# Kernel optimization log

Hardware: AMD Instinct MI355X
Metric: run time of the kernel (lower is better)

Reference implementation:

```python
import jax, jax.numpy as jnp
import numpy as np

DIM = 1024
HEADS = 16


def setup_inputs() -> dict:
    key = jax.random.key(0)
    k1, k2, k3, k4 = jax.random.split(key, 4)
    x = jax.random.normal(k1, (4, 2048, DIM), dtype=jnp.float32)
    # torch nn.Linear weights: [out_features, in_features]
    w_qkv = jax.random.normal(k2, (3 * DIM, DIM), dtype=jnp.float32) * (DIM ** -0.5)
    w_out = jax.random.normal(k3, (DIM, DIM), dtype=jnp.float32) * (DIM ** -0.5)
    b_out = jax.random.normal(k4, (DIM,), dtype=jnp.float32) * 0.01
    return {"x": x, "w_qkv": w_qkv, "w_out": w_out, "b_out": b_out}


def reference(x, w_qkv, w_out, b_out):
    b, n, d = x.shape
    h = HEADS
    hd = d // h
    scale = d ** -0.5  # note: full dim, matching the original module
    qkv = jnp.einsum('bnd,ed->bne', x, w_qkv)  # [b, n, 3d]
    q, k, v = jnp.split(qkv, 3, axis=-1)
    def to_heads(t):
        return t.reshape(b, n, h, hd).transpose(0, 2, 1, 3)  # [b, h, n, hd]
    q, k, v = map(to_heads, (q, k, v))
    dots = jnp.einsum('bhqd,bhkd->bhqk', q, k) * scale  # [b, h, n, n]
    attn = jax.nn.softmax(dots, axis=-1)
    out = jnp.einsum('bhqk,bhkd->bhqd', attn, v)  # [b, h, n, hd]
    out = out.transpose(0, 2, 1, 3).reshape(b, n, d)
    return jnp.einsum('bnd,ed->bne', out, w_out) + b_out
```

## Files before the change

### kernel.cpp

```cpp
#include <hip/hip_runtime.h>
#include <stdint.h>

#define SEQ   2048
#define NDIM  1024
#define NH    16
#define HD    64
#define KDIM  1024

typedef short  short8  __attribute__((ext_vector_type(8)));
typedef float  floatx4 __attribute__((ext_vector_type(4)));
typedef unsigned short ushort4v __attribute__((ext_vector_type(4)));
typedef _Float16 half8 __attribute__((ext_vector_type(8)));
typedef __fp16  fp16x2 __attribute__((ext_vector_type(2)));
typedef unsigned int uint4v __attribute__((ext_vector_type(4)));

typedef __attribute__((address_space(1))) void GV;
typedef __attribute__((address_space(3))) void LV;

#define QSCALE 0.04508422003f

__device__ __forceinline__ unsigned short f2bf(float f) {
    unsigned int u = __float_as_uint(f);
    u += 0x7fffu + ((u >> 16) & 1u);
    return (unsigned short)(u >> 16);
}

__device__ __forceinline__ float ex2(float x) {
#if __has_builtin(__builtin_amdgcn_exp2f)
    return __builtin_amdgcn_exp2f(x);
#else
    return exp2f(x);
#endif
}

__global__ __launch_bounds__(256) void cast_f32_bf16(const float* __restrict__ in,
                                                     unsigned short* __restrict__ out) {
    int i = (blockIdx.x * 256 + threadIdx.x) * 4;
    float4 v = *(const float4*)(in + i);
    ushort4v o;
    o.x = f2bf(v.x); o.y = f2bf(v.y); o.z = f2bf(v.z); o.w = f2bf(v.w);
    *(ushort4v*)(out + i) = o;
}

template<int MODE>
__global__ __launch_bounds__(256, 3)
void gemm_bt(const unsigned short* __restrict__ A,
             const unsigned short* __restrict__ B,
             unsigned short* __restrict__ Cq,
             unsigned short* __restrict__ Ck,
             unsigned short* __restrict__ Cv,
             const float* __restrict__ bias,
             float* __restrict__ Cout)
{
    __shared__ unsigned short As[128 * 32];
    __shared__ unsigned short Bs[128 * 32];
    const int tid  = threadIdx.x;
    const int lane = tid & 63;
    const int w    = tid >> 6;
    const int quad = lane >> 4;
    const int l15  = lane & 15;
    const int wm   = w >> 1, wn = w & 1;
    const int bm   = blockIdx.x, bn = blockIdx.y;

    const unsigned short* Arow = A + (size_t)bm * 128 * KDIM;
    const unsigned short* Brow = B + (size_t)bn * 128 * KDIM;

    const unsigned short* ga[2]; const unsigned short* gb[2];
    unsigned short* la[2];       unsigned short* lb[2];
#pragma unroll
    for (int i = 0; i < 2; ++i) {
        int j = ((w * 2 + i) << 6) + lane;
        int r = j >> 2;
        int c = (j & 3) ^ ((r >> 1) & 3);
        ga[i] = Arow + r * KDIM + c * 8;
        gb[i] = Brow + r * KDIM + c * 8;
        la[i] = (unsigned short*)As + ((w * 2 + i) << 9);
        lb[i] = (unsigned short*)Bs + ((w * 2 + i) << 9);
    }

    int achunk[4], bchunk[4];
#pragma unroll
    for (int t = 0; t < 4; ++t) {
        int ra = wm * 64 + t * 16 + l15;
        achunk[t] = (ra << 2) + (quad ^ ((ra >> 1) & 3));
        int rb = wn * 64 + t * 16 + l15;
        bchunk[t] = (rb << 2) + (quad ^ ((rb >> 1) & 3));
    }

    floatx4 acc[4][4];
#pragma unroll
    for (int mt = 0; mt < 4; ++mt)
#pragma unroll
        for (int nt = 0; nt < 4; ++nt)
            acc[mt][nt] = (floatx4){0.f, 0.f, 0.f, 0.f};

    for (int kt = 0; kt < KDIM / 32; ++kt) {
#pragma unroll
        for (int i = 0; i < 2; ++i) {
            __builtin_amdgcn_global_load_lds((GV*)(void*)(ga[i] + kt * 32), (LV*)(void*)la[i], 16, 0, 0);
            __builtin_amdgcn_global_load_lds((GV*)(void*)(gb[i] + kt * 32), (LV*)(void*)lb[i], 16, 0, 0);
        }
        __syncthreads();
        short8 af[4], bf[4];
#pragma unroll
        for (int t = 0; t < 4; ++t) {
            af[t] = *(const short8*)(As + (achunk[t] << 3));
            bf[t] = *(const short8*)(Bs + (bchunk[t] << 3));
        }
#pragma unroll
        for (int mt = 0; mt < 4; ++mt)
#pragma unroll
            for (int nt = 0; nt < 4; ++nt)
                acc[mt][nt] = __builtin_amdgcn_mfma_f32_16x16x32_bf16(af[mt], bf[nt], acc[mt][nt], 0, 0, 0);
        __syncthreads();
    }

    if (MODE == 0) {
        const int which = bn >> 3;
        unsigned short* dst = which == 0 ? Cq : (which == 1 ? Ck : Cv);
#pragma unroll
        for (int nt = 0; nt < 4; ++nt) {
            int e0   = ((bn & 7) << 7) + wn * 64 + nt * 16;
            int head = e0 >> 6;
            int hdi  = (e0 & 63) + l15;
#pragma unroll
            for (int mt = 0; mt < 4; ++mt) {
#pragma unroll
                for (int r = 0; r < 4; ++r) {
                    int m = bm * 128 + wm * 64 + mt * 16 + quad * 4 + r;
                    int b = m >> 11, n = m & 2047;
                    int bh = (b << 4) + head;
                    float val = acc[mt][nt][r];
                    if (which == 0) {
                        dst[((size_t)bh * SEQ + n) * HD + hdi] = f2bf(val * QSCALE);
                    } else if (which == 1) {
                        size_t idx = (size_t)bh * 131072
                                   + (size_t)(n >> 7) * 8192
                                   + (size_t)((((n >> 4) & 7) * 2) + (hdi >> 5)) * 512
                                   + ((((hdi >> 3) & 3) * 16) + (n & 15)) * 8
                                   + (hdi & 7);
                        dst[idx] = f2bf(val);
                    } else {
                        int nt7 = n & 127;
                        int u   = nt7 >> 5;
                        int k5  = nt7 & 31;
                        int c   = k5 & 15;
                        int q   = c >> 2;
                        int j   = ((k5 >> 4) << 2) | (c & 3);
                        size_t idx = (size_t)bh * 131072
                                   + (size_t)(n >> 7) * 8192
                                   + (size_t)(u * 4 + ((hdi >> 4) & 3)) * 512
                                   + (q * 16 + (hdi & 15)) * 8
                                   + j;
                        _Float16 hv = (_Float16)val;
                        dst[idx] = __builtin_bit_cast(unsigned short, hv);
                    }
                }
            }
        }
    } else {
#pragma unroll
        for (int nt = 0; nt < 4; ++nt) {
            int e = bn * 128 + wn * 64 + nt * 16 + l15;
            float bv = bias[e];
#pragma unroll
            for (int mt = 0; mt < 4; ++mt) {
#pragma unroll
                for (int r = 0; r < 4; ++r) {
                    int m = bm * 128 + wm * 64 + mt * 16 + quad * 4 + r;
                    Cout[(size_t)m * NDIM + e] = acc[mt][nt][r] + bv;
                }
            }
        }
    }
}

__global__ __launch_bounds__(256, 4)
void attn_fused(const unsigned short* __restrict__ qb,
                const unsigned short* __restrict__ kfrag,
                const unsigned short* __restrict__ vfrag,
                unsigned short* __restrict__ ob)
{
    __shared__ unsigned short Ks[8192];
    __shared__ unsigned short Vs[8192];

    const int tid  = threadIdx.x;
    const int lane = tid & 63;
    const int w    = tid >> 6;
    const int quad = lane >> 4;
    const int l15  = lane & 15;

    const int bid  = blockIdx.x;
    const int xcd  = bid & 7;
    const int slot = bid >> 3;
    const int bh   = xcd * 8 + (slot >> 4);
    const int q0   = (slot & 15) * 128;

    const unsigned short* Qb = qb    + (size_t)bh * SEQ * HD;
    const unsigned short* Kb = kfrag + (size_t)bh * 131072;
    const unsigned short* Vb = vfrag + (size_t)bh * 131072;

    short8 qf[2][2];
#pragma unroll
    for (int qt = 0; qt < 2; ++qt)
#pragma unroll
        for (int ks = 0; ks < 2; ++ks)
            qf[qt][ks] = *(const short8*)(Qb + (size_t)(q0 + w * 32 + qt * 16 + l15) * HD + ks * 32 + quad * 8);

    floatx4 oacc[2][4];
    floatx4 lacc4[2];
#pragma unroll
    for (int qt = 0; qt < 2; ++qt) {
#pragma unroll
        for (int nt = 0; nt < 4; ++nt) oacc[qt][nt] = (floatx4){0.f, 0.f, 0.f, 0.f};
        lacc4[qt] = (floatx4){0.f, 0.f, 0.f, 0.f};
    }
    half8 vones;
#pragma unroll
    for (int i = 0; i < 8; ++i) vones[i] = (_Float16)1.0f;

    const unsigned short* gk[4]; const unsigned short* gv[4];
    unsigned short* lk[4];       unsigned short* lv[4];
#pragma unroll
    for (int i = 0; i < 4; ++i) {
        int chunk = ((w * 4 + i) << 6) + lane;
        gk[i] = Kb + chunk * 8;
        gv[i] = Vb + chunk * 8;
        lk[i] = (unsigned short*)Ks + ((w * 4 + i) << 9) + lane * 8;
        lv[i] = (unsigned short*)Vs + ((w * 4 + i) << 9) + lane * 8;
    }

    uint4v pk[4], pv[4];
#pragma unroll
    for (int i = 0; i < 4; ++i) {
        pk[i] = *(const uint4v*)gk[i];
        pv[i] = *(const uint4v*)gv[i];
    }

    for (int kt = 0; kt < 16; ++kt) {
#pragma unroll
        for (int i = 0; i < 4; ++i) {
            *(uint4v*)lk[i] = pk[i];
            *(uint4v*)lv[i] = pv[i];
        }
        __syncthreads();
        if (kt < 15) {
#pragma unroll
            for (int i = 0; i < 4; ++i) {
                pk[i] = *(const uint4v*)(gk[i] + (kt + 1) * 8192);
                pv[i] = *(const uint4v*)(gv[i] + (kt + 1) * 8192);
            }
        }

        floatx4 sacc[2][8];
#pragma unroll
        for (int qt = 0; qt < 2; ++qt)
#pragma unroll
            for (int nt = 0; nt < 8; ++nt) sacc[qt][nt] = (floatx4){0.f, 0.f, 0.f, 0.f};
#pragma unroll
        for (int ks = 0; ks < 2; ++ks) {
#pragma unroll
            for (int nt = 0; nt < 8; ++nt) {
                short8 kf = *(const short8*)(Ks + (nt * 2 + ks) * 512 + lane * 8);
                sacc[0][nt] = __builtin_amdgcn_mfma_f32_16x16x32_bf16(kf, qf[0][ks], sacc[0][nt], 0, 0, 0);
                sacc[1][nt] = __builtin_amdgcn_mfma_f32_16x16x32_bf16(kf, qf[1][ks], sacc[1][nt], 0, 0, 0);
            }
        }

#pragma unroll
        for (int u = 0; u < 4; ++u) {
            half8 pf[2];
#pragma unroll
            for (int qt = 0; qt < 2; ++qt) {
                floatx4 s0 = sacc[qt][2 * u];
                floatx4 s1 = sacc[qt][2 * u + 1];
                fp16x2 c0 = __builtin_amdgcn_cvt_pkrtz(ex2(s0[0]), ex2(s0[1]));
                fp16x2 c1 = __builtin_amdgcn_cvt_pkrtz(ex2(s0[2]), ex2(s0[3]));
                fp16x2 c2 = __builtin_amdgcn_cvt_pkrtz(ex2(s1[0]), ex2(s1[1]));
                fp16x2 c3 = __builtin_amdgcn_cvt_pkrtz(ex2(s1[2]), ex2(s1[3]));
                uint4v uu;
                uu.x = __builtin_bit_cast(unsigned int, c0);
                uu.y = __builtin_bit_cast(unsigned int, c1);
                uu.z = __builtin_bit_cast(unsigned int, c2);
                uu.w = __builtin_bit_cast(unsigned int, c3);
                pf[qt] = __builtin_bit_cast(half8, uu);
                lacc4[qt] = __builtin_amdgcn_mfma_f32_16x16x32_f16(pf[qt], vones, lacc4[qt], 0, 0, 0);
            }
#pragma unroll
            for (int nt = 0; nt < 4; ++nt) {
                uint4v vv = *(const uint4v*)((const unsigned short*)Vs + (u * 4 + nt) * 512 + lane * 8);
                half8 vf = __builtin_bit_cast(half8, vv);
                oacc[0][nt] = __builtin_amdgcn_mfma_f32_16x16x32_f16(pf[0], vf, oacc[0][nt], 0, 0, 0);
                oacc[1][nt] = __builtin_amdgcn_mfma_f32_16x16x32_f16(pf[1], vf, oacc[1][nt], 0, 0, 0);
            }
        }
        __syncthreads();
    }

    const int b = bh >> 4, h = bh & 15;
#pragma unroll
    for (int qt = 0; qt < 2; ++qt) {
#pragma unroll
        for (int r = 0; r < 4; ++r) {
            float inv = 1.f / lacc4[qt][r];
            int n = q0 + w * 32 + qt * 16 + quad * 4 + r;
            size_t rowoff = ((size_t)b * SEQ + n) * NDIM + h * HD;
#pragma unroll
            for (int nt = 0; nt < 4; ++nt)
                ob[rowoff + nt * 16 + l15] = f2bf(oacc[qt][nt][r] * inv);
        }
    }
}

extern "C" void kernel_launch(void* const* d_in, const int* in_sizes, int n_in,
                              void* d_out, int out_size, void* d_ws, size_t ws_size,
                              hipStream_t stream)
{
    (void)in_sizes; (void)n_in; (void)out_size; (void)ws_size;
    const float* x    = (const float*)d_in[0];
    const float* wqkv = (const float*)d_in[1];
    const float* wout = (const float*)d_in[2];
    const float* bout = (const float*)d_in[3];
    float* out = (float*)d_out;

    unsigned short* xb    = (unsigned short*)d_ws;
    unsigned short* wqkvb = xb    + 8388608;
    unsigned short* woutb = wqkvb + 3145728;
    unsigned short* qbuf  = woutb + 1048576;
    unsigned short* kbuf  = qbuf  + 8388608;
    unsigned short* vbuf  = kbuf  + 8388608;
    unsigned short* obuf  = vbuf  + 8388608;

    cast_f32_bf16<<<8192, 256, 0, stream>>>(x, xb);
    cast_f32_bf16<<<3072, 256, 0, stream>>>(wqkv, wqkvb);
    cast_f32_bf16<<<1024, 256, 0, stream>>>(wout, woutb);

    gemm_bt<0><<<dim3(64, 24), 256, 0, stream>>>(xb, wqkvb, qbuf, kbuf, vbuf, nullptr, nullptr);
    attn_fused<<<1024, 256, 0, stream>>>(qbuf, kbuf, vbuf, obuf);
    gemm_bt<1><<<dim3(64, 8), 256, 0, stream>>>(obuf, woutb, nullptr, nullptr, nullptr, bout, out);
}
```

Measured before the change: 295.0 us.

## Double-buffer attention K/V tiles via async global-to-LDS loads; vectorize V epilogue stores

```diff
diff --git a/kernel.cpp b/kernel.cpp
--- a/kernel.cpp
+++ b/kernel.cpp
@@ -12,6 +12,7 @@
 typedef unsigned short ushort4v __attribute__((ext_vector_type(4)));
 typedef _Float16 half8 __attribute__((ext_vector_type(8)));
 typedef __fp16  fp16x2 __attribute__((ext_vector_type(2)));
+typedef unsigned int uint2v __attribute__((ext_vector_type(2)));
 typedef unsigned int uint4v __attribute__((ext_vector_type(4)));
 
 typedef __attribute__((address_space(1))) void GV;
@@ -118,42 +119,56 @@
     if (MODE == 0) {
         const int which = bn >> 3;
         unsigned short* dst = which == 0 ? Cq : (which == 1 ? Ck : Cv);
-#pragma unroll
-        for (int nt = 0; nt < 4; ++nt) {
-            int e0   = ((bn & 7) << 7) + wn * 64 + nt * 16;
-            int head = e0 >> 6;
-            int hdi  = (e0 & 63) + l15;
-#pragma unroll
-            for (int mt = 0; mt < 4; ++mt) {
-#pragma unroll
-                for (int r = 0; r < 4; ++r) {
-                    int m = bm * 128 + wm * 64 + mt * 16 + quad * 4 + r;
-                    int b = m >> 11, n = m & 2047;
+        if (which == 2) {
+#pragma unroll
+            for (int nt = 0; nt < 4; ++nt) {
+                int e0   = ((bn & 7) << 7) + wn * 64 + nt * 16;
+                int head = e0 >> 6;
+                int hdi  = (e0 & 63) + l15;
+#pragma unroll
+                for (int mt = 0; mt < 4; ++mt) {
+                    int n0 = bm * 128 + wm * 64 + mt * 16 + quad * 4;
+                    int b  = n0 >> 11;
+                    int n  = n0 & 2047;
                     int bh = (b << 4) + head;
-                    float val = acc[mt][nt][r];
-                    if (which == 0) {
-                        dst[((size_t)bh * SEQ + n) * HD + hdi] = f2bf(val * QSCALE);
-                    } else if (which == 1) {
-                        size_t idx = (size_t)bh * 131072
-                                   + (size_t)(n >> 7) * 8192
-                                   + (size_t)((((n >> 4) & 7) * 2) + (hdi >> 5)) * 512
-                                   + ((((hdi >> 3) & 3) * 16) + (n & 15)) * 8
-                                   + (hdi & 7);
-                        dst[idx] = f2bf(val);
-                    } else {
-                        int nt7 = n & 127;
-                        int u   = nt7 >> 5;
-                        int k5  = nt7 & 31;
-                        int c   = k5 & 15;
-                        int q   = c >> 2;
-                        int j   = ((k5 >> 4) << 2) | (c & 3);
-                        size_t idx = (size_t)bh * 131072
-                                   + (size_t)(n >> 7) * 8192
-                                   + (size_t)(u * 4 + ((hdi >> 4) & 3)) * 512
-                                   + (q * 16 + (hdi & 15)) * 8
-                                   + j;
-                        _Float16 hv = (_Float16)val;
-                        dst[idx] = __builtin_bit_cast(unsigned short, hv);
+                    int u  = (n & 127) >> 5;
+                    size_t base = (size_t)bh * 131072
+                                + (size_t)(n >> 7) * 8192
+                                + (size_t)(u * 4 + ((hdi >> 4) & 3)) * 512
+                                + (quad * 16 + (hdi & 15)) * 8
+                                + ((mt & 1) << 2);
+                    fp16x2 p01 = __builtin_amdgcn_cvt_pkrtz(acc[mt][nt][0], acc[mt][nt][1]);
+                    fp16x2 p23 = __builtin_amdgcn_cvt_pkrtz(acc[mt][nt][2], acc[mt][nt][3]);
+                    uint2v st;
+                    st.x = __builtin_bit_cast(unsigned int, p01);
+                    st.y = __builtin_bit_cast(unsigned int, p23);
+                    *(uint2v*)(dst + base) = st;
+                }
+            }
+        } else {
+#pragma unroll
+            for (int nt = 0; nt < 4; ++nt) {
+                int e0   = ((bn & 7) << 7) + wn * 64 + nt * 16;
+                int head = e0 >> 6;
+                int hdi  = (e0 & 63) + l15;
+#pragma unroll
+                for (int mt = 0; mt < 4; ++mt) {
+#pragma unroll
+                    for (int r = 0; r < 4; ++r) {
+                        int m = bm * 128 + wm * 64 + mt * 16 + quad * 4 + r;
+                        int b = m >> 11, n = m & 2047;
+                        int bh = (b << 4) + head;
+                        float val = acc[mt][nt][r];
+                        if (which == 0) {
+                            dst[((size_t)bh * SEQ + n) * HD + hdi] = f2bf(val * QSCALE);
+                        } else {
+                            size_t idx = (size_t)bh * 131072
+                                       + (size_t)(n >> 7) * 8192
+                                       + (size_t)((((n >> 4) & 7) * 2) + (hdi >> 5)) * 512
+                                       + ((((hdi >> 3) & 3) * 16) + (n & 15)) * 8
+                                       + (hdi & 7);
+                            dst[idx] = f2bf(val);
+                        }
                     }
                 }
             }
@@ -181,8 +196,8 @@
                 const unsigned short* __restrict__ vfrag,
                 unsigned short* __restrict__ ob)
 {
-    __shared__ unsigned short Ks[8192];
-    __shared__ unsigned short Vs[8192];
+    __shared__ unsigned short Ks[2][4096];
+    __shared__ unsigned short Vs[2][4096];
 
     const int tid  = threadIdx.x;
     const int lane = tid & 63;
@@ -219,56 +234,56 @@
 #pragma unroll
     for (int i = 0; i < 8; ++i) vones[i] = (_Float16)1.0f;
 
-    const unsigned short* gk[4]; const unsigned short* gv[4];
-    unsigned short* lk[4];       unsigned short* lv[4];
-#pragma unroll
-    for (int i = 0; i < 4; ++i) {
-        int chunk = ((w * 4 + i) << 6) + lane;
-        gk[i] = Kb + chunk * 8;
-        gv[i] = Vb + chunk * 8;
-        lk[i] = (unsigned short*)Ks + ((w * 4 + i) << 9) + lane * 8;
-        lv[i] = (unsigned short*)Vs + ((w * 4 + i) << 9) + lane * 8;
-    }
-
-    uint4v pk[4], pv[4];
-#pragma unroll
-    for (int i = 0; i < 4; ++i) {
-        pk[i] = *(const uint4v*)gk[i];
-        pv[i] = *(const uint4v*)gv[i];
-    }
-
-    for (int kt = 0; kt < 16; ++kt) {
-#pragma unroll
-        for (int i = 0; i < 4; ++i) {
-            *(uint4v*)lk[i] = pk[i];
-            *(uint4v*)lv[i] = pv[i];
-        }
+    const unsigned short* gk[2]; const unsigned short* gv[2];
+    unsigned short* lk[2][2];    unsigned short* lv[2][2];
+#pragma unroll
+    for (int i = 0; i < 2; ++i) {
+        int off = (((w * 2 + i) << 6) + lane) * 8;
+        gk[i] = Kb + off;
+        gv[i] = Vb + off;
+#pragma unroll
+        for (int b = 0; b < 2; ++b) {
+            lk[b][i] = &Ks[b][(w * 2 + i) << 9];
+            lv[b][i] = &Vs[b][(w * 2 + i) << 9];
+        }
+    }
+
+#pragma unroll
+    for (int i = 0; i < 2; ++i) {
+        __builtin_amdgcn_global_load_lds((GV*)(void*)gk[i], (LV*)(void*)lk[0][i], 16, 0, 0);
+        __builtin_amdgcn_global_load_lds((GV*)(void*)gv[i], (LV*)(void*)lv[0][i], 16, 0, 0);
+    }
+
+    for (int t = 0; t < 32; ++t) {
+        const int buf = t & 1;
         __syncthreads();
-        if (kt < 15) {
-#pragma unroll
-            for (int i = 0; i < 4; ++i) {
-                pk[i] = *(const uint4v*)(gk[i] + (kt + 1) * 8192);
-                pv[i] = *(const uint4v*)(gv[i] + (kt + 1) * 8192);
-            }
-        }
-
-        floatx4 sacc[2][8];
+        if (t < 31) {
+#pragma unroll
+            for (int i = 0; i < 2; ++i) {
+                __builtin_amdgcn_global_load_lds((GV*)(void*)(gk[i] + (t + 1) * 4096), (LV*)(void*)lk[buf ^ 1][i], 16, 0, 0);
+                __builtin_amdgcn_global_load_lds((GV*)(void*)(gv[i] + (t + 1) * 4096), (LV*)(void*)lv[buf ^ 1][i], 16, 0, 0);
+            }
+        }
+        const unsigned short* KsB = Ks[buf];
+        const unsigned short* VsB = Vs[buf];
+
+        floatx4 sacc[2][4];
 #pragma unroll
         for (int qt = 0; qt < 2; ++qt)
 #pragma unroll
-            for (int nt = 0; nt < 8; ++nt) sacc[qt][nt] = (floatx4){0.f, 0.f, 0.f, 0.f};
+            for (int nt = 0; nt < 4; ++nt) sacc[qt][nt] = (floatx4){0.f, 0.f, 0.f, 0.f};
 #pragma unroll
         for (int ks = 0; ks < 2; ++ks) {
 #pragma unroll
-            for (int nt = 0; nt < 8; ++nt) {
-                short8 kf = *(const short8*)(Ks + (nt * 2 + ks) * 512 + lane * 8);
+            for (int nt = 0; nt < 4; ++nt) {
+                short8 kf = *(const short8*)(KsB + (nt * 2 + ks) * 512 + lane * 8);
                 sacc[0][nt] = __builtin_amdgcn_mfma_f32_16x16x32_bf16(kf, qf[0][ks], sacc[0][nt], 0, 0, 0);
                 sacc[1][nt] = __builtin_amdgcn_mfma_f32_16x16x32_bf16(kf, qf[1][ks], sacc[1][nt], 0, 0, 0);
             }
         }
 
 #pragma unroll
-        for (int u = 0; u < 4; ++u) {
+        for (int u = 0; u < 2; ++u) {
             half8 pf[2];
 #pragma unroll
             for (int qt = 0; qt < 2; ++qt) {
@@ -288,13 +303,12 @@
             }
 #pragma unroll
             for (int nt = 0; nt < 4; ++nt) {
-                uint4v vv = *(const uint4v*)((const unsigned short*)Vs + (u * 4 + nt) * 512 + lane * 8);
+                uint4v vv = *(const uint4v*)(VsB + (u * 4 + nt) * 512 + lane * 8);
                 half8 vf = __builtin_bit_cast(half8, vv);
                 oacc[0][nt] = __builtin_amdgcn_mfma_f32_16x16x32_f16(pf[0], vf, oacc[0][nt], 0, 0, 0);
                 oacc[1][nt] = __builtin_amdgcn_mfma_f32_16x16x32_f16(pf[1], vf, oacc[1][nt], 0, 0, 0);
             }
         }
-        __syncthreads();
     }
 
     const int b = bh >> 4, h = bh & 15;
```

Measured after the change: 261.0 us. 11.5% less time.
